# Kernel tuning notes

Hardware: AMD Instinct MI355X
Metric: run time of the kernel (lower is better)

Reference implementation:

```python
import jax, jax.numpy as jnp
import numpy as np

B, N, C, H = 1, 256, 128, 4
DH = C // H  # per-head dim = 32
KEY_SCALE = DH ** -0.5


def setup_inputs() -> dict:
    key = jax.random.key(0)
    ks = jax.random.split(key, 9)
    return {
        "q_data": jax.random.normal(ks[0], (B, N, N, C), jnp.float32),
        "m_data": jax.random.normal(ks[1], (B, N, N, C), jnp.float32),
        "bias": jax.random.normal(ks[2], (B, N, 1, 1, N), jnp.float32),
        "nonbatched_bias": jax.random.normal(ks[3], (1, H, N, N), jnp.float32),
        "wq": jax.random.normal(ks[4], (C, C), jnp.float32) * (1.0 / np.sqrt(C)),
        "wk": jax.random.normal(ks[5], (C, C), jnp.float32) * (1.0 / np.sqrt(C)),
        "wv": jax.random.normal(ks[6], (C, C), jnp.float32) * (1.0 / np.sqrt(C)),
        "wo": jax.random.normal(ks[7], (C, C), jnp.float32) * (1.0 / np.sqrt(C)),
        "bo": jnp.zeros((C,), jnp.float32),
        "wg": jax.random.normal(ks[8], (C, C), jnp.float32) * (1.0 / np.sqrt(C)),
        "bg": jnp.ones((C,), jnp.float32),
    }


def reference(q_data, m_data, bias, nonbatched_bias, wq, wk, wv, wo, bo, wg, bg):
    # projections (torch Linear: x @ W.T), weights stored [out, in]
    q = (q_data @ wq.T) * KEY_SCALE            # [B, N, Nq, H*DH]
    k = m_data @ wk.T                          # [B, N, Nk, H*DH]
    v = m_data @ wv.T                          # [B, N, Nk, H*DH]
    q = q.reshape(B, N, N, H, DH)
    k = k.reshape(B, N, N, H, DH)
    v = v.reshape(B, N, N, H, DH)
    # logits: [B, N, H, Nq, Nk]
    logits = jnp.einsum("bnqhd,bnkhd->bnhqk", q, k)
    logits = logits + bias + nonbatched_bias   # bias [B,N,1,1,Nk]; nb [1,H,Nq,Nk]
    weight = jax.nn.softmax(logits, axis=-1)
    wa = jnp.einsum("bnhqk,bnkhd->bnqhd", weight, v)  # [B, N, Nq, H, DH]
    g = jax.nn.sigmoid(q_data @ wg.T + bg).reshape(B, N, N, H, DH)
    wa = wa * g
    out = wa.reshape(B, N, N, H * DH) @ wo.T + bo
    return out
```

## Files before the change

### kernel.cpp

```cpp
#include <hip/hip_runtime.h>
#include <hip/hip_bf16.h>

typedef unsigned short u16;
typedef unsigned int u32;

#define N_ 256
#define C_ 128
#define H_ 4
#define DH_ 32
#define R_ (N_*N_)

static constexpr float KEY_SCALE_ = 0.17677669529663687f;

typedef __attribute__((ext_vector_type(8))) short bf16x8;
typedef __attribute__((ext_vector_type(4))) float f32x4;

__device__ __forceinline__ float bf2f(u16 b){ return __uint_as_float(((u32)b)<<16); }
__device__ __forceinline__ u16 f2bf(float f){
  u32 u = __float_as_uint(f);
  u += 0x7FFFu + ((u>>16)&1u);
  return (u16)(u>>16);
}
__device__ __forceinline__ u32 pack2bf(float lo, float hi){
  return (u32)f2bf(lo) | ((u32)f2bf(hi) << 16);
}

__global__ __launch_bounds__(256) void wconv_kernel(
    const float* __restrict__ wq, const float* __restrict__ wk,
    const float* __restrict__ wv, const float* __restrict__ wg,
    u16* __restrict__ wtb)
{
  int id = blockIdx.x*256 + threadIdx.x;
  int m = id >> 12;
  int e = (id & 4095)*4;
  const float* src = (m==0) ? wq : (m==1) ? wk : (m==2) ? wv : wg;
  const float4 v = *(const float4*)(src + e);
  const float s = (m==0) ? KEY_SCALE_ : 1.f;
  ushort4 o;
  o.x = f2bf(v.x*s); o.y = f2bf(v.y*s); o.z = f2bf(v.z*s); o.w = f2bf(v.w*s);
  *(ushort4*)(wtb + m*16384 + e) = o;
}

__global__ __launch_bounds__(256) void nbtr_kernel(
    const float* __restrict__ nb, float* __restrict__ nbT)
{
  __shared__ float T[64][65];
  const int t = threadIdx.x;
  const int q0 = (blockIdx.x & 3)*64, k0 = (blockIdx.x >> 2)*64;
  const int h = blockIdx.y;
  const float* src = nb + (size_t)h*N_*N_;
  float* dst = nbT + (size_t)h*N_*N_;
  #pragma unroll
  for (int p=0;p<16;p++){
    int id = t + p*256;
    int r = id >> 6, cc = id & 63;
    T[cc][r] = src[(size_t)(q0 + r)*N_ + k0 + cc];
  }
  __syncthreads();
  #pragma unroll
  for (int p=0;p<16;p++){
    int id = t + p*256;
    int r = id >> 6, cc = id & 63;
    dst[(size_t)(k0 + r)*N_ + q0 + cc] = T[r][cc];
  }
}

#define XSTR 136
__global__ __launch_bounds__(256, 2) void proj_kernel(
    const float* __restrict__ qd, const float* __restrict__ md,
    const u16* __restrict__ wtb, const float* __restrict__ bg,
    u16* __restrict__ qb, u16* __restrict__ kb,
    u16* __restrict__ vb, u16* __restrict__ gb)
{
  __shared__ u16 Xs[256*XSTR];
  const int t = threadIdx.x;
  const int y = blockIdx.y;
  const size_t row0 = (size_t)blockIdx.x * 256;
  const float* X = y ? md : qd;

  #pragma unroll
  for (int p=0;p<16;p++){
    int id = t + p*256;
    int r = id >> 4, c0 = (id & 15)*8;
    const float* s = X + (row0 + r)*C_ + c0;
    float4 a = *(const float4*)s;
    float4 b = *(const float4*)(s+4);
    uint2 w0; w0.x = pack2bf(a.x, a.y); w0.y = pack2bf(a.z, a.w);
    uint2 w1; w1.x = pack2bf(b.x, b.y); w1.y = pack2bf(b.z, b.w);
    *(uint2*)&Xs[r*XSTR + c0]     = w0;
    *(uint2*)&Xs[r*XSTR + c0 + 4] = w1;
  }

  const int w = t >> 6, l = t & 63, c = l & 15, g = l >> 4;
  const int matSel = w >> 1;
  const int ctBase = (w & 1) * 4;
  const int matIdx = y ? (matSel ? 2 : 1) : (matSel ? 3 : 0);
  u16* dst = y ? (matSel ? vb : kb) : (matSel ? gb : qb);
  const bool doSig = (!y) && matSel;

  bf16x8 bfr[4][4];
  {
    const u16* wb = wtb + matIdx*16384;
    #pragma unroll
    for (int ctj=0;ctj<4;ctj++){
      const u16* rp = wb + ((ctBase+ctj)*16 + c)*C_ + g*8;
      #pragma unroll
      for (int kk=0;kk<4;kk++)
        bfr[ctj][kk] = *(const bf16x8*)(rp + kk*32);
    }
  }
  float bgv[4];
  if (doSig){
    #pragma unroll
    for (int ctj=0;ctj<4;ctj++) bgv[ctj] = bg[(ctBase+ctj)*16 + c];
  }
  __syncthreads();

  for (int mt=0; mt<16; mt++){
    bf16x8 af[4];
    #pragma unroll
    for (int kk=0;kk<4;kk++)
      af[kk] = *(const bf16x8*)&Xs[(mt*16 + c)*XSTR + kk*32 + g*8];
    f32x4 a0 = {0.f,0.f,0.f,0.f}, a1 = {0.f,0.f,0.f,0.f};
    f32x4 a2 = {0.f,0.f,0.f,0.f}, a3 = {0.f,0.f,0.f,0.f};
    #pragma unroll
    for (int kk=0;kk<4;kk++){
      a0 = __builtin_amdgcn_mfma_f32_16x16x32_bf16(af[kk], bfr[0][kk], a0, 0,0,0);
      a1 = __builtin_amdgcn_mfma_f32_16x16x32_bf16(af[kk], bfr[1][kk], a1, 0,0,0);
      a2 = __builtin_amdgcn_mfma_f32_16x16x32_bf16(af[kk], bfr[2][kk], a2, 0,0,0);
      a3 = __builtin_amdgcn_mfma_f32_16x16x32_bf16(af[kk], bfr[3][kk], a3, 0,0,0);
    }
    f32x4 accs[4] = {a0,a1,a2,a3};
    #pragma unroll
    for (int ctj=0;ctj<4;ctj++){
      #pragma unroll
      for (int r=0;r<4;r++){
        float v = accs[ctj][r];
        if (doSig) v = 1.f/(1.f+__expf(-(v + bgv[ctj])));
        dst[(row0 + mt*16 + 4*g + r)*C_ + (ctBase+ctj)*16 + c] = f2bf(v);
      }
    }
  }
}

#define VSTR 264
__global__ __launch_bounds__(256) void attn_kernel(
    const u16* qb, const u16* __restrict__ kb,
    const u16* __restrict__ vb, const u16* __restrict__ gb,
    const float* __restrict__ bias, const float* __restrict__ nbT,
    u16* wab)
{
  __shared__ u16 Vt[32*VSTR];
  __shared__ u16 Ps[16*VSTR];
  __shared__ float Om[4][16][36];
  __shared__ float Red[4][16];
  __shared__ float Bs[256];

  const int t  = threadIdx.x;
  const int h  = blockIdx.x;
  const int n  = blockIdx.y;
  const int w  = t >> 6;
  const int l  = t & 63;
  const int c  = l & 15;
  const int g  = l >> 4;

  {
    const u16* vsrc = vb + ((size_t)n*N_)*C_ + h*DH_;
    for (int idx = t; idx < 1024; idx += 256){
      int k = idx >> 2, ch = idx & 3;
      int sk = (k & ~31) | ((k & 15) << 1) | ((k >> 4) & 1);
      ushort4 a = *(const ushort4*)(vsrc + (size_t)k*C_ + ch*8);
      ushort4 b = *(const ushort4*)(vsrc + (size_t)k*C_ + ch*8 + 4);
      u16 e[8] = {(u16)a.x,(u16)a.y,(u16)a.z,(u16)a.w,
                  (u16)b.x,(u16)b.y,(u16)b.z,(u16)b.w};
      int d0 = ch*8;
      #pragma unroll
      for (int jj=0;jj<8;jj++){
        int d = d0 + jj;
        int vr = (d&1)*16 + (d>>1);
        Vt[vr*VSTR + sk] = e[jj];
      }
    }
    Bs[t] = bias[(size_t)n*N_ + t];
  }
  __syncthreads();

  bf16x8 kf[4];
  float bsv[4];
  {
    const u16* kbase = kb + ((size_t)(n*N_ + c))*C_ + h*DH_ + g*8;
    #pragma unroll
    for (int j=0;j<4;j++){
      kf[j] = *(const bf16x8*)(kbase + (size_t)(4*w + j)*16*C_);
      bsv[j] = Bs[(4*w + j)*16 + c];
    }
  }

  bf16x8 onesb;
  #pragma unroll
  for (int i=0;i<8;i++) onesb[i] = (short)0x3F80;

  const float* nbtp = nbT + (size_t)h*N_*N_;
  const u16* qbase = qb + ((size_t)(n*N_ + c))*C_ + h*DH_ + g*8;

  bf16x8 af = *(const bf16x8*)qbase;

  for (int it=0; it<16; ++it){
    const int q0 = it*16;

    f32x4 acc[4];
    #pragma unroll
    for (int j=0;j<4;j++){
      const int kt = 4*w + j;
      const float4 nb4 = *(const float4*)(nbtp + (size_t)(kt*16 + c)*N_ + q0 + 4*g);
      f32x4 ci;
      ci[0] = bsv[j] + nb4.x; ci[1] = bsv[j] + nb4.y;
      ci[2] = bsv[j] + nb4.z; ci[3] = bsv[j] + nb4.w;
      acc[j] = __builtin_amdgcn_mfma_f32_16x16x32_bf16(af, kf[j], ci, 0, 0, 0);
    }

    #pragma unroll
    for (int j=0;j<4;j++){
      #pragma unroll
      for (int r=0;r<4;r++) acc[j][r] = __expf(acc[j][r]);
    }

    #pragma unroll
    for (int r=0;r<4;r++){
      *(u32*)&Ps[(4*g+r)*VSTR + 64*w + 2*c]      = pack2bf(acc[0][r], acc[1][r]);
      *(u32*)&Ps[(4*g+r)*VSTR + 64*w + 32 + 2*c] = pack2bf(acc[2][r], acc[3][r]);
    }

    f32x4 o0 = {0.f,0.f,0.f,0.f}, o1 = {0.f,0.f,0.f,0.f};
    f32x4 o2 = {0.f,0.f,0.f,0.f};
    #pragma unroll
    for (int ss=0;ss<2;ss++){
      const int s = 2*w + ss;
      bf16x8 pa = *(const bf16x8*)&Ps[c*VSTR + s*32 + g*8];
      bf16x8 v0 = *(const bf16x8*)&Vt[(size_t)c*VSTR      + s*32 + g*8];
      bf16x8 v1 = *(const bf16x8*)&Vt[(size_t)(16+c)*VSTR + s*32 + g*8];
      o0 = __builtin_amdgcn_mfma_f32_16x16x32_bf16(pa, v0, o0, 0, 0, 0);
      o1 = __builtin_amdgcn_mfma_f32_16x16x32_bf16(pa, v1, o1, 0, 0, 0);
      o2 = __builtin_amdgcn_mfma_f32_16x16x32_bf16(pa, onesb, o2, 0, 0, 0);
    }

    bf16x8 afn = af;
    if (it < 15) afn = *(const bf16x8*)(qbase + (size_t)(q0 + 16)*C_);

    if (c==0){
      #pragma unroll
      for (int r=0;r<4;r++) Red[w][4*g+r] = o2[r];
    }
    #pragma unroll
    for (int r=0;r<4;r++){
      Om[w][4*g+r][c]      = o0[r];
      Om[w][4*g+r][16 + c] = o1[r];
    }
    __syncthreads();

    {
      const int q = 4*g + w;
      float sum = (Red[0][q] + Red[1][q]) + (Red[2][q] + Red[3][q]);
      float inv = 1.f/sum;
      float od0 = (Om[0][q][c]    + Om[1][q][c])    + (Om[2][q][c]    + Om[3][q][c]);
      float od1 = (Om[0][q][16+c] + Om[1][q][16+c]) + (Om[2][q][16+c] + Om[3][q][16+c]);
      size_t row = (size_t)n*N_ + q0 + q;
      u32 g2 = *(const u32*)&gb[row*C_ + h*DH_ + 2*c];
      float g0v = bf2f((u16)(g2 & 0xFFFFu));
      float g1v = bf2f((u16)(g2 >> 16));
      *(u32*)&wab[row*C_ + h*DH_ + 2*c] = pack2bf(od0*inv*g0v, od1*inv*g1v);
    }
    __syncthreads();
    af = afn;
  }
}

#define WSTR 136
__global__ __launch_bounds__(256, 2) void outproj_kernel(
    const u16* __restrict__ wab, const float* __restrict__ wo,
    const float* __restrict__ bo, float* __restrict__ out)
{
  __shared__ u16 Wos[128*WSTR];
  const int t = threadIdx.x;
  const size_t row0 = (size_t)blockIdx.x * 128;

  #pragma unroll
  for (int p=0;p<8;p++){
    int id = t + p*256;
    int r = id >> 4, c0 = (id & 15)*8;
    const float* s = wo + r*C_ + c0;
    float4 a = *(const float4*)s;
    float4 b = *(const float4*)(s+4);
    uint2 w0; w0.x = pack2bf(a.x, a.y); w0.y = pack2bf(a.z, a.w);
    uint2 w1; w1.x = pack2bf(b.x, b.y); w1.y = pack2bf(b.z, b.w);
    *(uint2*)&Wos[r*WSTR + c0]     = w0;
    *(uint2*)&Wos[r*WSTR + c0 + 4] = w1;
  }

  const int w = t >> 6, l = t & 63, c = l & 15, g = l >> 4;

  bf16x8 af[2][4];
  #pragma unroll
  for (int mt=0;mt<2;mt++){
    const u16* ap = wab + (row0 + w*32 + mt*16 + c)*C_ + g*8;
    #pragma unroll
    for (int kk=0;kk<4;kk++)
      af[mt][kk] = *(const bf16x8*)(ap + kk*32);
  }
  __syncthreads();

  for (int ct=0;ct<8;ct++){
    bf16x8 bfr[4];
    #pragma unroll
    for (int kk=0;kk<4;kk++)
      bfr[kk] = *(const bf16x8*)&Wos[(ct*16 + c)*WSTR + kk*32 + g*8];
    f32x4 acc0 = {0.f,0.f,0.f,0.f}, acc1 = {0.f,0.f,0.f,0.f};
    #pragma unroll
    for (int kk=0;kk<4;kk++){
      acc0 = __builtin_amdgcn_mfma_f32_16x16x32_bf16(af[0][kk], bfr[kk], acc0, 0,0,0);
      acc1 = __builtin_amdgcn_mfma_f32_16x16x32_bf16(af[1][kk], bfr[kk], acc1, 0,0,0);
    }
    const float bov = bo[ct*16 + c];
    #pragma unroll
    for (int r=0;r<4;r++){
      out[(row0 + w*32 +      4*g + r)*C_ + ct*16 + c] = acc0[r] + bov;
      out[(row0 + w*32 + 16 + 4*g + r)*C_ + ct*16 + c] = acc1[r] + bov;
    }
  }
}

extern "C" void kernel_launch(void* const* d_in, const int* in_sizes, int n_in,
                              void* d_out, int out_size, void* d_ws, size_t ws_size,
                              hipStream_t stream) {
  const float* qd   = (const float*)d_in[0];
  const float* md   = (const float*)d_in[1];
  const float* bias = (const float*)d_in[2];
  const float* nb   = (const float*)d_in[3];
  const float* wq   = (const float*)d_in[4];
  const float* wk   = (const float*)d_in[5];
  const float* wv   = (const float*)d_in[6];
  const float* wo   = (const float*)d_in[7];
  const float* bo   = (const float*)d_in[8];
  const float* wg   = (const float*)d_in[9];
  const float* bg   = (const float*)d_in[10];
  float* out = (float*)d_out;

  char* ws = (char*)d_ws;
  const size_t MB16 = (size_t)16*1024*1024;
  u16* qb  = (u16*)(ws);
  u16* kb  = (u16*)(ws + MB16);
  u16* vb  = (u16*)(ws + 2*MB16);
  u16* gb  = (u16*)(ws + 3*MB16);
  u16* wab = qb;
  u16*   wtb = (u16*)d_out;
  float* nbT = (float*)((char*)d_out + 131072);

  wconv_kernel<<<64, 256, 0, stream>>>(wq, wk, wv, wg, wtb);
  nbtr_kernel<<<dim3(16, 4), 256, 0, stream>>>(nb, nbT);
  proj_kernel<<<dim3(256, 2), 256, 0, stream>>>(qd, md, wtb, bg, qb, kb, vb, gb);
  attn_kernel<<<dim3(H_, N_), 256, 0, stream>>>(qb, kb, vb, gb, bias, nbT, wab);
  outproj_kernel<<<512, 256, 0, stream>>>(wab, wo, bo, out);
}
```

Baseline: 105.7 us.

## Merge prep kernels, double-buffer attention reduction, prefetch bias and gate loads

Merges the weight conversion and non-batched-bias transpose into one launch, removing a kernel launch. The attention loop now double-buffers its shared reduction buffers to drop one barrier per iteration. It also prefetches the next iteration's nbT and q tiles, plus the gate values, ahead of the softmax and PV MFMAs. Partial outputs are stored in LDS as packed bf16, which halves LDS traffic but adds rounding error before the cross-wave sum. Bias values are read straight from global memory, and bf16 conversion now uses the HIP intrinsics.

```diff
diff --git a/kernel.cpp b/kernel.cpp
--- a/kernel.cpp
+++ b/kernel.cpp
@@ -17,51 +17,53 @@
 
 __device__ __forceinline__ float bf2f(u16 b){ return __uint_as_float(((u32)b)<<16); }
 __device__ __forceinline__ u16 f2bf(float f){
-  u32 u = __float_as_uint(f);
-  u += 0x7FFFu + ((u>>16)&1u);
-  return (u16)(u>>16);
+  __hip_bfloat16 h = __float2bfloat16(f);
+  u16 r; __builtin_memcpy(&r, &h, 2); return r;
 }
 __device__ __forceinline__ u32 pack2bf(float lo, float hi){
-  return (u32)f2bf(lo) | ((u32)f2bf(hi) << 16);
-}
-
-__global__ __launch_bounds__(256) void wconv_kernel(
+  __hip_bfloat162 h2 = __float22bfloat162_rn(make_float2(lo, hi));
+  u32 r; __builtin_memcpy(&r, &h2, 4); return r;
+}
+
+__global__ __launch_bounds__(256) void prep_kernel(
     const float* __restrict__ wq, const float* __restrict__ wk,
     const float* __restrict__ wv, const float* __restrict__ wg,
-    u16* __restrict__ wtb)
-{
-  int id = blockIdx.x*256 + threadIdx.x;
-  int m = id >> 12;
-  int e = (id & 4095)*4;
-  const float* src = (m==0) ? wq : (m==1) ? wk : (m==2) ? wv : wg;
-  const float4 v = *(const float4*)(src + e);
-  const float s = (m==0) ? KEY_SCALE_ : 1.f;
-  ushort4 o;
-  o.x = f2bf(v.x*s); o.y = f2bf(v.y*s); o.z = f2bf(v.z*s); o.w = f2bf(v.w*s);
-  *(ushort4*)(wtb + m*16384 + e) = o;
-}
-
-__global__ __launch_bounds__(256) void nbtr_kernel(
-    const float* __restrict__ nb, float* __restrict__ nbT)
+    const float* __restrict__ nb,
+    u16* __restrict__ wtb, float* __restrict__ nbT)
 {
   __shared__ float T[64][65];
+  const int b = blockIdx.x;
   const int t = threadIdx.x;
-  const int q0 = (blockIdx.x & 3)*64, k0 = (blockIdx.x >> 2)*64;
-  const int h = blockIdx.y;
-  const float* src = nb + (size_t)h*N_*N_;
-  float* dst = nbT + (size_t)h*N_*N_;
-  #pragma unroll
-  for (int p=0;p<16;p++){
-    int id = t + p*256;
-    int r = id >> 6, cc = id & 63;
-    T[cc][r] = src[(size_t)(q0 + r)*N_ + k0 + cc];
-  }
-  __syncthreads();
-  #pragma unroll
-  for (int p=0;p<16;p++){
-    int id = t + p*256;
-    int r = id >> 6, cc = id & 63;
-    dst[(size_t)(k0 + r)*N_ + q0 + cc] = T[r][cc];
+  if (b < 64){
+    int id = b*256 + t;
+    int m = id >> 12;
+    int e = (id & 4095)*4;
+    const float* src = (m==0) ? wq : (m==1) ? wk : (m==2) ? wv : wg;
+    const float4 v = *(const float4*)(src + e);
+    const float s = (m==0) ? KEY_SCALE_ : 1.f;
+    uint2 o;
+    o.x = pack2bf(v.x*s, v.y*s);
+    o.y = pack2bf(v.z*s, v.w*s);
+    *(uint2*)(wtb + m*16384 + e) = o;
+  } else {
+    const int bb = b - 64;
+    const int q0 = (bb & 3)*64, k0 = ((bb >> 2) & 3)*64;
+    const int h = bb >> 4;
+    const float* src = nb + (size_t)h*N_*N_;
+    float* dst = nbT + (size_t)h*N_*N_;
+    #pragma unroll
+    for (int p=0;p<16;p++){
+      int id = t + p*256;
+      int r = id >> 6, cc = id & 63;
+      T[cc][r] = src[(size_t)(q0 + r)*N_ + k0 + cc];
+    }
+    __syncthreads();
+    #pragma unroll
+    for (int p=0;p<16;p++){
+      int id = t + p*256;
+      int r = id >> 6, cc = id & 63;
+      dst[(size_t)(k0 + r)*N_ + q0 + cc] = T[r][cc];
+    }
   }
 }
 
@@ -133,17 +135,26 @@
     f32x4 accs[4] = {a0,a1,a2,a3};
     #pragma unroll
     for (int ctj=0;ctj<4;ctj++){
+      float v[4];
       #pragma unroll
       for (int r=0;r<4;r++){
-        float v = accs[ctj][r];
-        if (doSig) v = 1.f/(1.f+__expf(-(v + bgv[ctj])));
-        dst[(row0 + mt*16 + 4*g + r)*C_ + (ctBase+ctj)*16 + c] = f2bf(v);
+        v[r] = accs[ctj][r];
+        if (doSig) v[r] = 1.f/(1.f+__expf(-(v[r] + bgv[ctj])));
       }
+      u32 pk01 = pack2bf(v[0], v[1]);
+      u32 pk23 = pack2bf(v[2], v[3]);
+      size_t rb = row0 + mt*16 + 4*g;
+      int col = (ctBase+ctj)*16 + c;
+      dst[(rb+0)*C_ + col] = (u16)pk01;
+      dst[(rb+1)*C_ + col] = (u16)(pk01 >> 16);
+      dst[(rb+2)*C_ + col] = (u16)pk23;
+      dst[(rb+3)*C_ + col] = (u16)(pk23 >> 16);
     }
   }
 }
 
 #define VSTR 264
+#define OMSTR 18
 __global__ __launch_bounds__(256) void attn_kernel(
     const u16* qb, const u16* __restrict__ kb,
     const u16* __restrict__ vb, const u16* __restrict__ gb,
@@ -152,9 +163,8 @@
 {
   __shared__ u16 Vt[32*VSTR];
   __shared__ u16 Ps[16*VSTR];
-  __shared__ float Om[4][16][36];
-  __shared__ float Red[4][16];
-  __shared__ float Bs[256];
+  __shared__ u32 Om[2][4][16*OMSTR];
+  __shared__ float Red[2][4][16];
 
   const int t  = threadIdx.x;
   const int h  = blockIdx.x;
@@ -181,7 +191,6 @@
         Vt[vr*VSTR + sk] = e[jj];
       }
     }
-    Bs[t] = bias[(size_t)n*N_ + t];
   }
   __syncthreads();
 
@@ -189,10 +198,11 @@
   float bsv[4];
   {
     const u16* kbase = kb + ((size_t)(n*N_ + c))*C_ + h*DH_ + g*8;
+    const float* brow = bias + (size_t)n*N_;
     #pragma unroll
     for (int j=0;j<4;j++){
       kf[j] = *(const bf16x8*)(kbase + (size_t)(4*w + j)*16*C_);
-      bsv[j] = Bs[(4*w + j)*16 + c];
+      bsv[j] = brow[(4*w + j)*16 + c];
     }
   }
 
@@ -204,20 +214,31 @@
   const u16* qbase = qb + ((size_t)(n*N_ + c))*C_ + h*DH_ + g*8;
 
   bf16x8 af = *(const bf16x8*)qbase;
+  float4 nb4[4];
+  #pragma unroll
+  for (int j=0;j<4;j++)
+    nb4[j] = *(const float4*)(nbtp + (size_t)((4*w+j)*16 + c)*N_ + 4*g);
 
   for (int it=0; it<16; ++it){
+    const int p  = it & 1;
     const int q0 = it*16;
 
     f32x4 acc[4];
     #pragma unroll
     for (int j=0;j<4;j++){
-      const int kt = 4*w + j;
-      const float4 nb4 = *(const float4*)(nbtp + (size_t)(kt*16 + c)*N_ + q0 + 4*g);
       f32x4 ci;
-      ci[0] = bsv[j] + nb4.x; ci[1] = bsv[j] + nb4.y;
-      ci[2] = bsv[j] + nb4.z; ci[3] = bsv[j] + nb4.w;
+      ci[0] = bsv[j] + nb4[j].x; ci[1] = bsv[j] + nb4[j].y;
+      ci[2] = bsv[j] + nb4[j].z; ci[3] = bsv[j] + nb4[j].w;
       acc[j] = __builtin_amdgcn_mfma_f32_16x16x32_bf16(af, kf[j], ci, 0, 0, 0);
     }
+
+    const int q0n = (it < 15) ? q0 + 16 : q0;
+    #pragma unroll
+    for (int j=0;j<4;j++)
+      nb4[j] = *(const float4*)(nbtp + (size_t)((4*w+j)*16 + c)*N_ + q0n + 4*g);
+    bf16x8 afn = *(const bf16x8*)(qbase + (size_t)q0n*C_);
+    const size_t mrow = (size_t)n*N_ + q0 + 4*g + w;
+    u32 g2 = *(const u32*)&gb[mrow*C_ + h*DH_ + 2*c];
 
     #pragma unroll
     for (int j=0;j<4;j++){
@@ -244,33 +265,31 @@
       o2 = __builtin_amdgcn_mfma_f32_16x16x32_bf16(pa, onesb, o2, 0, 0, 0);
     }
 
-    bf16x8 afn = af;
-    if (it < 15) afn = *(const bf16x8*)(qbase + (size_t)(q0 + 16)*C_);
-
     if (c==0){
       #pragma unroll
-      for (int r=0;r<4;r++) Red[w][4*g+r] = o2[r];
-    }
-    #pragma unroll
-    for (int r=0;r<4;r++){
-      Om[w][4*g+r][c]      = o0[r];
-      Om[w][4*g+r][16 + c] = o1[r];
-    }
+      for (int r=0;r<4;r++) Red[p][w][4*g+r] = o2[r];
+    }
+    #pragma unroll
+    for (int r=0;r<4;r++)
+      Om[p][w][(4*g+r)*OMSTR + c] = pack2bf(o0[r], o1[r]);
+
     __syncthreads();
 
     {
       const int q = 4*g + w;
-      float sum = (Red[0][q] + Red[1][q]) + (Red[2][q] + Red[3][q]);
+      float sum = (Red[p][0][q] + Red[p][1][q]) + (Red[p][2][q] + Red[p][3][q]);
       float inv = 1.f/sum;
-      float od0 = (Om[0][q][c]    + Om[1][q][c])    + (Om[2][q][c]    + Om[3][q][c]);
-      float od1 = (Om[0][q][16+c] + Om[1][q][16+c]) + (Om[2][q][16+c] + Om[3][q][16+c]);
-      size_t row = (size_t)n*N_ + q0 + q;
-      u32 g2 = *(const u32*)&gb[row*C_ + h*DH_ + 2*c];
+      float od0 = 0.f, od1 = 0.f;
+      #pragma unroll
+      for (int w2=0;w2<4;w2++){
+        u32 v = Om[p][w2][q*OMSTR + c];
+        od0 += bf2f((u16)(v & 0xFFFFu));
+        od1 += bf2f((u16)(v >> 16));
+      }
       float g0v = bf2f((u16)(g2 & 0xFFFFu));
       float g1v = bf2f((u16)(g2 >> 16));
-      *(u32*)&wab[row*C_ + h*DH_ + 2*c] = pack2bf(od0*inv*g0v, od1*inv*g1v);
-    }
-    __syncthreads();
+      *(u32*)&wab[mrow*C_ + h*DH_ + 2*c] = pack2bf(od0*inv*g0v, od1*inv*g1v);
+    }
     af = afn;
   }
 }
@@ -355,8 +374,7 @@
   u16*   wtb = (u16*)d_out;
   float* nbT = (float*)((char*)d_out + 131072);
 
-  wconv_kernel<<<64, 256, 0, stream>>>(wq, wk, wv, wg, wtb);
-  nbtr_kernel<<<dim3(16, 4), 256, 0, stream>>>(nb, nbT);
+  prep_kernel<<<128, 256, 0, stream>>>(wq, wk, wv, wg, nb, wtb, nbT);
   proj_kernel<<<dim3(256, 2), 256, 0, stream>>>(qd, md, wtb, bg, qb, kb, vb, gb);
   attn_kernel<<<dim3(H_, N_), 256, 0, stream>>>(qb, kb, vb, gb, bias, nbT, wab);
   outproj_kernel<<<512, 256, 0, stream>>>(wab, wo, bo, out);
```

Result: no change. 104.2 us (-1.4%).
